# Optimization experiments

Hardware: AMD Instinct MI355X
Metric: run time of the kernel (lower is better)

Reference implementation:

```python
import jax, jax.numpy as jnp
import numpy as np
from jax import lax

Z_DIM, X_DIM, Y_DIM, H_DIM = 128, 64, 64, 512


def setup_inputs() -> dict:
    key = jax.random.key(0)
    ks = jax.random.split(key, 10)
    s = 1.0 / np.sqrt(H_DIM)
    inp = {
        "z": jax.random.normal(ks[0], (1024, Z_DIM), dtype=jnp.float32),
        "x": jax.random.normal(ks[1], (1024, 32, X_DIM), dtype=jnp.float32),
        # LSTM params (PyTorch layout: gates ordered i,f,g,o)
        "W_ih": jax.random.uniform(ks[2], (4 * H_DIM, X_DIM), jnp.float32, -s, s),
        "W_hh": jax.random.uniform(ks[3], (4 * H_DIM, H_DIM), jnp.float32, -s, s),
        "b_ih": jax.random.uniform(ks[4], (4 * H_DIM,), jnp.float32, -s, s),
        "b_hh": jax.random.uniform(ks[5], (4 * H_DIM,), jnp.float32, -s, s),
        # proj_network: z_dim -> hidden
        "W_proj": jax.random.uniform(ks[6], (H_DIM, Z_DIM), jnp.float32, -s, s),
        "b_proj": jax.random.uniform(ks[7], (H_DIM,), jnp.float32, -s, s),
        # projout_network: hidden -> y_dim
        "W_out": jax.random.uniform(ks[8], (Y_DIM, H_DIM), jnp.float32, -s, s),
        "b_out": jax.random.uniform(ks[9], (Y_DIM,), jnp.float32, -s, s),
        "y_pred_len": 128,
    }
    return inp


def reference(z, x, W_ih, W_hh, b_ih, b_hh, W_proj, b_proj, W_out, b_out, y_pred_len):
    # initial recurrent state: h0 = c0 = proj(z)  [B, H]
    h0 = z @ W_proj.T + b_proj
    c0 = h0
    y_prev0 = x[:, -1, :]  # [B, X_DIM]

    def step(carry, _):
        h, c, y_prev = carry
        gates = y_prev @ W_ih.T + b_ih + h @ W_hh.T + b_hh  # [B, 4H]
        i, f, g, o = jnp.split(gates, 4, axis=-1)
        i = jax.nn.sigmoid(i)
        f = jax.nn.sigmoid(f)
        g = jnp.tanh(g)
        o = jax.nn.sigmoid(o)
        c = f * c + i * g
        h = o * jnp.tanh(c)
        y_cur = y_prev + (h @ W_out.T + b_out)  # residual (inference: feed back)
        return (h, c, y_cur), y_cur

    _, ys = lax.scan(step, (h0, c0, y_prev0), None, length=y_pred_len)
    return jnp.transpose(ys, (1, 0, 2))  # [B, T, Y_DIM]
```

## Files before the change

### kernel.cpp

```cpp
#include <hip/hip_runtime.h>
#include <stdint.h>

typedef _Float16 half8 __attribute__((ext_vector_type(8)));
typedef __attribute__((ext_vector_type(4))) float f4;
typedef __attribute__((ext_vector_type(4))) unsigned int u32x4;
typedef __attribute__((ext_vector_type(2))) unsigned int u32x2;

#define LDAH 200
#define EXS  36
#define HSTR 40

__device__ __forceinline__ float sigm(float x) { return 1.0f / (1.0f + __expf(-x)); }
__device__ __forceinline__ float tanh_(float x) { return 1.0f - 2.0f / (__expf(2.0f * x) + 1.0f); }


extern "C" __global__ void __launch_bounds__(256) k_wcat(
    const float* __restrict__ Wih, const float* __restrict__ Whh,
    _Float16* __restrict__ WA, _Float16* __restrict__ WB)
{
    int idx = blockIdx.x * 256 + threadIdx.x;
    int n = idx / 576, k = idx % 576;
    float v = (k < 64) ? Wih[n * 64 + k] : Whh[n * 512 + (k - 64)];
    _Float16 b = (_Float16)v;
    WA[idx] = b;
    if (k < 64) WB[idx] = b;
}

extern "C" __global__ void __launch_bounds__(256) k_comb(
    const float* __restrict__ Wih, const float* __restrict__ Whh,
    const float* __restrict__ Wo, _Float16* __restrict__ WB)
{
    int bx = blockIdx.x;
    int n = bx >> 1;
    int kh = ((bx & 1) << 8) + threadIdx.x;
    float acc = Whh[n * 512 + kh];
    #pragma unroll 16
    for (int p = 0; p < 64; ++p)
        acc += Wih[n * 64 + p] * Wo[p * 512 + kh];
    WB[n * 576 + 64 + kh] = (_Float16)acc;
}

extern "C" __global__ void __launch_bounds__(256) k_misc(
    const float* __restrict__ Wo, const float* __restrict__ bih, const float* __restrict__ bhh,
    const float* __restrict__ Wih, const float* __restrict__ bo, const float* __restrict__ x,
    _Float16* __restrict__ WoB, float* __restrict__ b0v, float* __restrict__ b1v,
    float* __restrict__ yf0, float* __restrict__ yf1,
    _Float16* __restrict__ yh0, _Float16* __restrict__ yh1,
    _Float16* __restrict__ yl0, _Float16* __restrict__ yl1)
{
    int idx = blockIdx.x * 256 + threadIdx.x;
    if (idx < 32768) { WoB[idx] = (_Float16)Wo[idx]; return; }
    if (idx < 34816) {
        int n = idx - 32768;
        float b = bih[n] + bhh[n];
        b0v[n] = b;
        float a = b;
        #pragma unroll 16
        for (int p = 0; p < 64; ++p) a += Wih[n * 64 + p] * bo[p];
        b1v[n] = a;
        return;
    }
    if (idx < 100352) {
        int e = idx - 34816;
        int m = e >> 6, nn = e & 63;
        float v = x[m * 2048 + 31 * 64 + nn];
        yf0[e] = v; yf1[e] = v;
        _Float16 hi = (_Float16)v;
        _Float16 lo = (_Float16)(v - (float)hi);
        yh0[e] = hi; yh1[e] = hi;
        yl0[e] = lo; yl1[e] = lo;
    }
}

extern "C" __global__ void __launch_bounds__(256) k_h0(
    const float* __restrict__ z, const float* __restrict__ Wp, const float* __restrict__ bp,
    float* __restrict__ cst, _Float16* __restrict__ hh0, _Float16* __restrict__ hl0)
{
    int bx = blockIdx.x;
    int m = bx >> 1;
    int n = ((bx & 1) << 8) + threadIdx.x;
    float acc = bp[n];
    const f4* zr = (const f4*)&z[m * 128];
    const f4* wr = (const f4*)&Wp[n * 128];
    #pragma unroll 8
    for (int p = 0; p < 32; ++p) {
        f4 zv = zr[p], wv = wr[p];
        acc += zv[0]*wv[0] + zv[1]*wv[1] + zv[2]*wv[2] + zv[3]*wv[3];
    }
    cst[m * 512 + n] = acc;
    _Float16 hi = (_Float16)acc;
    hh0[m * 512 + n] = hi;
    hl0[m * 512 + n] = (_Float16)(acc - (float)hi);
}


__device__ __forceinline__ void resolve_y(
    int t, int row, int c4,
    const float* __restrict__ yf_in, float* __restrict__ yf_out,
    const float* __restrict__ dl_in, const float* __restrict__ bout,
    _Float16* __restrict__ yh_out, _Float16* __restrict__ yl_out,
    float* __restrict__ out)
{
    f4 a = *(const f4*)&yf_in[row * 64 + c4];
    a += *(const f4*)&bout[c4];
    #pragma unroll
    for (int sp = 0; sp < 16; ++sp)
        a += *(const f4*)&dl_in[sp * 65536 + row * 64 + c4];
    *(f4*)&yf_out[row * 64 + c4] = a;
    *(f4*)&out[row * 8192 + (t - 1) * 64 + c4] = a;
    _Float16 hi4[4], lo4[4];
    #pragma unroll
    for (int x = 0; x < 4; ++x) {
        hi4[x] = (_Float16)a[x];
        lo4[x] = (_Float16)(a[x] - (float)hi4[x]);
    }
    *(u32x2*)&yh_out[row * 64 + c4] = *(u32x2*)hi4;
    *(u32x2*)&yl_out[row * 64 + c4] = *(u32x2*)lo4;
}

extern "C" __global__ void __launch_bounds__(512, 2) k_step(
    int t,
    const _Float16* __restrict__ Wcat,
    const float* __restrict__ bias,
    const _Float16* __restrict__ Wout,
    const float* __restrict__ bout,
    const _Float16* __restrict__ hh_in, const _Float16* __restrict__ hl_in,
    _Float16* __restrict__ hh_out, _Float16* __restrict__ hl_out,
    float* __restrict__ cst,
    const float* __restrict__ yf_in, float* __restrict__ yf_out,
    const _Float16* __restrict__ yh_in, _Float16* __restrict__ yh_out,
    const _Float16* __restrict__ yl_in, _Float16* __restrict__ yl_out,
    const float* __restrict__ dl_in, float* __restrict__ dl_out,
    float* __restrict__ out)
{
    __shared__ __align__(16) unsigned char smem[61440];
    _Float16* sAh = (_Float16*)smem;
    _Float16* sAl = (_Float16*)(smem + 25600);
    float*    sEx = (float*)smem;
    _Float16* sHh = (_Float16*)(smem + 51200);
    _Float16* sHl = (_Float16*)(smem + 56320);

    const int tid = threadIdx.x;
    const int bx  = blockIdx.x;
    const int mt  = bx >> 4, s = bx & 15;
    const int m0  = mt * 64, j0 = s * 32;

    if (t >= 128) {
        if (tid < 64) {
            int row = m0 + s * 4 + (tid >> 4);
            int c4  = (tid & 15) * 4;
            resolve_y(t, row, c4, yf_in, yf_out, dl_in, bout, yh_out, yl_out, out);
        }
        return;
    }

    const int w = tid >> 6, lane = tid & 63, l15 = lane & 15, quad = lane >> 4;
    const int quad8 = quad * 8;
    const int q = w >> 1, hx = w & 1;

    const int cm = tid >> 3, cjb = (tid & 7) * 4;
    const int cjcol = j0 + cjb;
    const int ccrow = (m0 + cm) * 512 + cjcol;
    f4 cpre = *(const f4*)&cst[ccrow];
    f4 bi0 = *(const f4*)&bias[       cjcol];
    f4 bi1 = *(const f4*)&bias[ 512 + cjcol];
    f4 bi2 = *(const f4*)&bias[1024 + cjcol];
    f4 bi3 = *(const f4*)&bias[1536 + cjcol];
    const int dn = w >> 1, ap = w & 1;
    half8 bw = *(const half8*)&Wout[(dn * 16 + l15) * 512 + j0 + quad8];

    const int brow = (q * 512 + j0 + hx * 16 + l15) * 576;

    half8 bv[2][6];
    #pragma unroll
    for (int kc = 0; kc < 6; ++kc)
        bv[0][kc] = *(const half8*)&Wcat[brow + kc * 32 + quad8];

    int rr[3], cc3[3];
    #pragma unroll
    for (int it = 0; it < 3; ++it) {
        int i4 = it * 512 + tid;
        rr[it]  = i4 / 24;
        cc3[it] = (i4 % 24) * 8;
    }

    #pragma unroll
    for (int it = 0; it < 3; ++it) {
        int r = rr[it], cc = cc3[it];
        const _Float16 *sh, *sl;
        if (cc < 64) { sh = &yh_in[(m0 + r) * 64 + cc];         sl = &yl_in[(m0 + r) * 64 + cc]; }
        else         { sh = &hh_in[(m0 + r) * 512 + (cc - 64)]; sl = &hl_in[(m0 + r) * 512 + (cc - 64)]; }
        *(u32x4*)&sAh[r * LDAH + cc] = *(const u32x4*)sh;
        *(u32x4*)&sAl[r * LDAH + cc] = *(const u32x4*)sl;
    }

    f4 zero = {0.0f, 0.0f, 0.0f, 0.0f};
    f4 acc[4];
    acc[0] = zero; acc[1] = zero; acc[2] = zero; acc[3] = zero;

    u32x4 regH[3], regL[3];
    #pragma unroll
    for (int ch = 0; ch < 3; ++ch) {
        if (ch < 2) {
            #pragma unroll
            for (int it = 0; it < 3; ++it) {
                int c = (ch + 1) * 192 + cc3[it] - 64;
                regH[it] = *(const u32x4*)&hh_in[(m0 + rr[it]) * 512 + c];
                regL[it] = *(const u32x4*)&hl_in[(m0 + rr[it]) * 512 + c];
            }
            #pragma unroll
            for (int kc = 0; kc < 6; ++kc)
                bv[(ch + 1) & 1][kc] = *(const half8*)&Wcat[brow + (ch + 1) * 192 + kc * 32 + quad8];
        }
        __syncthreads();
        #pragma unroll
        for (int kc = 0; kc < 6; ++kc) {
            int kq = kc * 32 + quad8;
            half8 b = bv[ch & 1][kc];
            #pragma unroll
            for (int a = 0; a < 4; ++a) {
                half8 ah = *(const half8*)&sAh[(l15 + a * 16) * LDAH + kq];
                acc[a] = __builtin_amdgcn_mfma_f32_16x16x32_f16(ah, b, acc[a], 0, 0, 0);
            }
            #pragma unroll
            for (int a = 0; a < 4; ++a) {
                half8 al = *(const half8*)&sAl[(l15 + a * 16) * LDAH + kq];
                acc[a] = __builtin_amdgcn_mfma_f32_16x16x32_f16(al, b, acc[a], 0, 0, 0);
            }
        }
        if (ch < 2) {
            __syncthreads();
            #pragma unroll
            for (int it = 0; it < 3; ++it) {
                *(u32x4*)&sAh[rr[it] * LDAH + cc3[it]] = regH[it];
                *(u32x4*)&sAl[rr[it] * LDAH + cc3[it]] = regL[it];
            }
        }
    }
    __syncthreads();

    #pragma unroll
    for (int a = 0; a < 4; ++a)
        #pragma unroll
        for (int r = 0; r < 4; ++r)
            sEx[(q * 64 + a * 16 + quad * 4 + r) * EXS + hx * 16 + l15] = acc[a][r];
    __syncthreads();

    {
        f4 c0 = cpre;
        f4 gI = *(const f4*)&sEx[(0 * 64 + cm) * EXS + cjb];
        f4 gF = *(const f4*)&sEx[(1 * 64 + cm) * EXS + cjb];
        f4 gG = *(const f4*)&sEx[(2 * 64 + cm) * EXS + cjb];
        f4 gO = *(const f4*)&sEx[(3 * 64 + cm) * EXS + cjb];
        _Float16 hi4[4], lo4[4];
        #pragma unroll
        for (int x = 0; x < 4; ++x) {
            float iv = sigm(gI[x] + bi0[x]);
            float fv = sigm(gF[x] + bi1[x]);
            float gv = tanh_(gG[x] + bi2[x]);
            float ov = sigm(gO[x] + bi3[x]);
            float cn = fv * c0[x] + iv * gv;
            float hn = ov * tanh_(cn);
            c0[x] = cn;
            _Float16 hi = (_Float16)hn;
            hi4[x] = hi;
            lo4[x] = (_Float16)(hn - (float)hi);
        }
        *(f4*)&cst[ccrow] = c0;
        *(u32x2*)&hh_out[ccrow]        = *(u32x2*)hi4;
        *(u32x2*)&hl_out[ccrow]        = *(u32x2*)lo4;
        *(u32x2*)&sHh[cm * HSTR + cjb] = *(u32x2*)hi4;
        *(u32x2*)&sHl[cm * HSTR + cjb] = *(u32x2*)lo4;
    }
    __syncthreads();

    {
        f4 d[2];
        d[0] = zero; d[1] = zero;
        #pragma unroll
        for (int a2 = 0; a2 < 2; ++a2) {
            int a = ap * 2 + a2;
            half8 ahh = *(const half8*)&sHh[(a * 16 + l15) * HSTR + quad8];
            half8 ahl = *(const half8*)&sHl[(a * 16 + l15) * HSTR + quad8];
            d[a2] = __builtin_amdgcn_mfma_f32_16x16x32_f16(ahh, bw, d[a2], 0, 0, 0);
            d[a2] = __builtin_amdgcn_mfma_f32_16x16x32_f16(ahl, bw, d[a2], 0, 0, 0);
        }
        #pragma unroll
        for (int a2 = 0; a2 < 2; ++a2) {
            int a = ap * 2 + a2;
            #pragma unroll
            for (int r = 0; r < 4; ++r)
                dl_out[s * 65536 + (m0 + a * 16 + quad * 4 + r) * 64 + dn * 16 + l15] = d[a2][r];
        }
    }

    if (t >= 1 && tid < 64) {
        int row = m0 + s * 4 + (tid >> 4);
        int c4  = (tid & 15) * 4;
        resolve_y(t, row, c4, yf_in, yf_out, dl_in, bout, yh_out, yl_out, out);
    }
}

extern "C" void kernel_launch(void* const* d_in, const int* in_sizes, int n_in,
                              void* d_out, int out_size, void* d_ws, size_t ws_size,
                              hipStream_t stream)
{
    const float* z   = (const float*)d_in[0];
    const float* x   = (const float*)d_in[1];
    const float* Wih = (const float*)d_in[2];
    const float* Whh = (const float*)d_in[3];
    const float* bih = (const float*)d_in[4];
    const float* bhh = (const float*)d_in[5];
    const float* Wp  = (const float*)d_in[6];
    const float* bp  = (const float*)d_in[7];
    const float* Wo  = (const float*)d_in[8];
    const float* bo  = (const float*)d_in[9];

    char* w = (char*)d_ws;
    _Float16* WA  = (_Float16*)w; w += 2359296;
    _Float16* WB  = (_Float16*)w; w += 2359296;
    _Float16* WoB = (_Float16*)w; w += 65536;
    float* b0v = (float*)w; w += 8192;
    float* b1v = (float*)w; w += 8192;
    _Float16* hh[2];
    hh[0] = (_Float16*)w; w += 1048576;
    hh[1] = (_Float16*)w; w += 1048576;
    _Float16* hl[2];
    hl[0] = (_Float16*)w; w += 1048576;
    hl[1] = (_Float16*)w; w += 1048576;
    float* cst = (float*)w; w += 2097152;
    float* yf[2];
    yf[0] = (float*)w; w += 262144;
    yf[1] = (float*)w; w += 262144;
    _Float16* yh[2];
    yh[0] = (_Float16*)w; w += 131072;
    yh[1] = (_Float16*)w; w += 131072;
    _Float16* yl[2];
    yl[0] = (_Float16*)w; w += 131072;
    yl[1] = (_Float16*)w; w += 131072;
    float* dl[2];
    dl[0] = (float*)w; w += 4194304;
    dl[1] = (float*)w; w += 4194304;
    float* out = (float*)d_out;

    k_wcat<<<4608, 256, 0, stream>>>(Wih, Whh, WA, WB);
    k_comb<<<4096, 256, 0, stream>>>(Wih, Whh, Wo, WB);
    k_misc<<<392, 256, 0, stream>>>(Wo, bih, bhh, Wih, bo, x, WoB, b0v, b1v,
                                    yf[0], yf[1], yh[0], yh[1], yl[0], yl[1]);
    k_h0<<<2048, 256, 0, stream>>>(z, Wp, bp, cst, hh[0], hl[0]);

    for (int t = 0; t <= 128; ++t) {
        k_step<<<256, 512, 0, stream>>>(t,
            (t == 0) ? WA : WB, (t == 0) ? b0v : b1v,
            WoB, bo,
            hh[t & 1], hl[t & 1], hh[(t + 1) & 1], hl[(t + 1) & 1],
            cst,
            yf[t & 1], yf[(t + 1) & 1],
            yh[t & 1], yh[(t + 1) & 1],
            yl[t & 1], yl[(t + 1) & 1],
            dl[(t + 1) & 1], dl[t & 1],
            out);
    }
}
```

Measured before the change: 2.183 ms.

## Split step kernel into 512 narrower blocks with XCD-aware tile mapping

Halves the hidden-column slice per block (32 to 16) and the threads per block (512 to 256), doubling the grid to 512 blocks so more of the device's compute units are occupied. Block indices are remapped so the row tiles for one batch slice stay on the same XCD, which should improve L2 reuse of the shared activation reads. The y-resolve step is moved to the start of the kernel. The trade-off is that each block now reloads the full 64-row activation tile for half the output columns, and the partial-output buffer doubles to 32 slices that resolve_y must sum.

```diff
diff --git a/kernel.cpp b/kernel.cpp
--- a/kernel.cpp
+++ b/kernel.cpp
@@ -7,8 +7,8 @@
 typedef __attribute__((ext_vector_type(2))) unsigned int u32x2;
 
 #define LDAH 200
-#define EXS  36
-#define HSTR 40
+#define EXS2 20
+#define HST2 24
 
 __device__ __forceinline__ float sigm(float x) { return 1.0f / (1.0f + __expf(-x)); }
 __device__ __forceinline__ float tanh_(float x) { return 1.0f - 2.0f / (__expf(2.0f * x) + 1.0f); }
@@ -95,16 +95,16 @@
 
 
 __device__ __forceinline__ void resolve_y(
-    int t, int row, int c4,
+    int t, int row, int c4, f4 bo4,
     const float* __restrict__ yf_in, float* __restrict__ yf_out,
-    const float* __restrict__ dl_in, const float* __restrict__ bout,
+    const float* __restrict__ dl_in,
     _Float16* __restrict__ yh_out, _Float16* __restrict__ yl_out,
     float* __restrict__ out)
 {
     f4 a = *(const f4*)&yf_in[row * 64 + c4];
-    a += *(const f4*)&bout[c4];
-    #pragma unroll
-    for (int sp = 0; sp < 16; ++sp)
+    a += bo4;
+    #pragma unroll
+    for (int sp = 0; sp < 32; ++sp)
         a += *(const f4*)&dl_in[sp * 65536 + row * 64 + c4];
     *(f4*)&yf_out[row * 64 + c4] = a;
     *(f4*)&out[row * 8192 + (t - 1) * 64 + c4] = a;
@@ -118,7 +118,7 @@
     *(u32x2*)&yl_out[row * 64 + c4] = *(u32x2*)lo4;
 }
 
-extern "C" __global__ void __launch_bounds__(512, 2) k_step(
+extern "C" __global__ void __launch_bounds__(256, 2) k_step(
     int t,
     const _Float16* __restrict__ Wcat,
     const float* __restrict__ bias,
@@ -133,32 +133,32 @@
     const float* __restrict__ dl_in, float* __restrict__ dl_out,
     float* __restrict__ out)
 {
-    __shared__ __align__(16) unsigned char smem[61440];
+    __shared__ __align__(16) unsigned char smem[57344];
     _Float16* sAh = (_Float16*)smem;
     _Float16* sAl = (_Float16*)(smem + 25600);
     float*    sEx = (float*)smem;
     _Float16* sHh = (_Float16*)(smem + 51200);
-    _Float16* sHl = (_Float16*)(smem + 56320);
+    _Float16* sHl = (_Float16*)(smem + 54272);
 
     const int tid = threadIdx.x;
     const int bx  = blockIdx.x;
-    const int mt  = bx >> 4, s = bx & 15;
-    const int m0  = mt * 64, j0 = s * 32;
-
-    if (t >= 128) {
-        if (tid < 64) {
-            int row = m0 + s * 4 + (tid >> 4);
-            int c4  = (tid & 15) * 4;
-            resolve_y(t, row, c4, yf_in, yf_out, dl_in, bout, yh_out, yl_out, out);
-        }
-        return;
-    }
-
-    const int w = tid >> 6, lane = tid & 63, l15 = lane & 15, quad = lane >> 4;
+    const int xcd = bx & 7, slot = bx >> 3;
+    const int mt  = xcd * 2 + (slot >> 5);
+    const int s   = slot & 31;
+    const int m0  = mt * 64, j0 = s * 16;
+
+    if (t >= 1 && tid < 32) {
+        int row = m0 + s * 2 + (tid >> 4);
+        int c4  = (tid & 15) * 4;
+        f4 bo4 = *(const f4*)&bout[c4];
+        resolve_y(t, row, c4, bo4, yf_in, yf_out, dl_in, yh_out, yl_out, out);
+    }
+    if (t >= 128) return;
+
+    const int wv = tid >> 6, lane = tid & 63, l15 = lane & 15, quad = lane >> 4;
     const int quad8 = quad * 8;
-    const int q = w >> 1, hx = w & 1;
-
-    const int cm = tid >> 3, cjb = (tid & 7) * 4;
+
+    const int cm = tid >> 2, cjb = (tid & 3) * 4;
     const int cjcol = j0 + cjb;
     const int ccrow = (m0 + cm) * 512 + cjcol;
     f4 cpre = *(const f4*)&cst[ccrow];
@@ -166,27 +166,26 @@
     f4 bi1 = *(const f4*)&bias[ 512 + cjcol];
     f4 bi2 = *(const f4*)&bias[1024 + cjcol];
     f4 bi3 = *(const f4*)&bias[1536 + cjcol];
-    const int dn = w >> 1, ap = w & 1;
-    half8 bw = *(const half8*)&Wout[(dn * 16 + l15) * 512 + j0 + quad8];
-
-    const int brow = (q * 512 + j0 + hx * 16 + l15) * 576;
+    half8 bw = *(const half8*)&Wout[(wv * 16 + l15) * 512 + j0 + (quad & 1) * 8];
+
+    const int brow = (wv * 512 + j0 + l15) * 576;
 
     half8 bv[2][6];
     #pragma unroll
     for (int kc = 0; kc < 6; ++kc)
         bv[0][kc] = *(const half8*)&Wcat[brow + kc * 32 + quad8];
 
-    int rr[3], cc3[3];
-    #pragma unroll
-    for (int it = 0; it < 3; ++it) {
-        int i4 = it * 512 + tid;
+    int rr[6], cc6[6];
+    #pragma unroll
+    for (int it = 0; it < 6; ++it) {
+        int i4 = it * 256 + tid;
         rr[it]  = i4 / 24;
-        cc3[it] = (i4 % 24) * 8;
-    }
-
-    #pragma unroll
-    for (int it = 0; it < 3; ++it) {
-        int r = rr[it], cc = cc3[it];
+        cc6[it] = (i4 % 24) * 8;
+    }
+
+    #pragma unroll
+    for (int it = 0; it < 6; ++it) {
+        int r = rr[it], cc = cc6[it];
         const _Float16 *sh, *sl;
         if (cc < 64) { sh = &yh_in[(m0 + r) * 64 + cc];         sl = &yl_in[(m0 + r) * 64 + cc]; }
         else         { sh = &hh_in[(m0 + r) * 512 + (cc - 64)]; sl = &hl_in[(m0 + r) * 512 + (cc - 64)]; }
@@ -198,13 +197,13 @@
     f4 acc[4];
     acc[0] = zero; acc[1] = zero; acc[2] = zero; acc[3] = zero;
 
-    u32x4 regH[3], regL[3];
+    u32x4 regH[6], regL[6];
     #pragma unroll
     for (int ch = 0; ch < 3; ++ch) {
         if (ch < 2) {
             #pragma unroll
-            for (int it = 0; it < 3; ++it) {
-                int c = (ch + 1) * 192 + cc3[it] - 64;
+            for (int it = 0; it < 6; ++it) {
+                int c = (ch + 1) * 192 + cc6[it] - 64;
                 regH[it] = *(const u32x4*)&hh_in[(m0 + rr[it]) * 512 + c];
                 regL[it] = *(const u32x4*)&hl_in[(m0 + rr[it]) * 512 + c];
             }
@@ -231,9 +230,9 @@
         if (ch < 2) {
             __syncthreads();
             #pragma unroll
-            for (int it = 0; it < 3; ++it) {
-                *(u32x4*)&sAh[rr[it] * LDAH + cc3[it]] = regH[it];
-                *(u32x4*)&sAl[rr[it] * LDAH + cc3[it]] = regL[it];
+            for (int it = 0; it < 6; ++it) {
+                *(u32x4*)&sAh[rr[it] * LDAH + cc6[it]] = regH[it];
+                *(u32x4*)&sAl[rr[it] * LDAH + cc6[it]] = regL[it];
             }
         }
     }
@@ -243,15 +242,15 @@
     for (int a = 0; a < 4; ++a)
         #pragma unroll
         for (int r = 0; r < 4; ++r)
-            sEx[(q * 64 + a * 16 + quad * 4 + r) * EXS + hx * 16 + l15] = acc[a][r];
+            sEx[(wv * 64 + a * 16 + quad * 4 + r) * EXS2 + l15] = acc[a][r];
     __syncthreads();
 
     {
         f4 c0 = cpre;
-        f4 gI = *(const f4*)&sEx[(0 * 64 + cm) * EXS + cjb];
-        f4 gF = *(const f4*)&sEx[(1 * 64 + cm) * EXS + cjb];
-        f4 gG = *(const f4*)&sEx[(2 * 64 + cm) * EXS + cjb];
-        f4 gO = *(const f4*)&sEx[(3 * 64 + cm) * EXS + cjb];
+        f4 gI = *(const f4*)&sEx[(0 * 64 + cm) * EXS2 + cjb];
+        f4 gF = *(const f4*)&sEx[(1 * 64 + cm) * EXS2 + cjb];
+        f4 gG = *(const f4*)&sEx[(2 * 64 + cm) * EXS2 + cjb];
+        f4 gO = *(const f4*)&sEx[(3 * 64 + cm) * EXS2 + cjb];
         _Float16 hi4[4], lo4[4];
         #pragma unroll
         for (int x = 0; x < 4; ++x) {
@@ -269,35 +268,26 @@
         *(f4*)&cst[ccrow] = c0;
         *(u32x2*)&hh_out[ccrow]        = *(u32x2*)hi4;
         *(u32x2*)&hl_out[ccrow]        = *(u32x2*)lo4;
-        *(u32x2*)&sHh[cm * HSTR + cjb] = *(u32x2*)hi4;
-        *(u32x2*)&sHl[cm * HSTR + cjb] = *(u32x2*)lo4;
+        *(u32x2*)&sHh[cm * HST2 + cjb] = *(u32x2*)hi4;
+        *(u32x2*)&sHl[cm * HST2 + cjb] = *(u32x2*)lo4;
     }
     __syncthreads();
 
     {
-        f4 d[2];
-        d[0] = zero; d[1] = zero;
-        #pragma unroll
-        for (int a2 = 0; a2 < 2; ++a2) {
-            int a = ap * 2 + a2;
-            half8 ahh = *(const half8*)&sHh[(a * 16 + l15) * HSTR + quad8];
-            half8 ahl = *(const half8*)&sHl[(a * 16 + l15) * HSTR + quad8];
-            d[a2] = __builtin_amdgcn_mfma_f32_16x16x32_f16(ahh, bw, d[a2], 0, 0, 0);
-            d[a2] = __builtin_amdgcn_mfma_f32_16x16x32_f16(ahl, bw, d[a2], 0, 0, 0);
-        }
-        #pragma unroll
-        for (int a2 = 0; a2 < 2; ++a2) {
-            int a = ap * 2 + a2;
+        const _Float16* hsrc = (quad < 2) ? sHh : sHl;
+        f4 d[4];
+        #pragma unroll
+        for (int a = 0; a < 4; ++a) d[a] = zero;
+        #pragma unroll
+        for (int a = 0; a < 4; ++a) {
+            half8 av = *(const half8*)&hsrc[(a * 16 + l15) * HST2 + (quad & 1) * 8];
+            d[a] = __builtin_amdgcn_mfma_f32_16x16x32_f16(av, bw, d[a], 0, 0, 0);
+        }
+        #pragma unroll
+        for (int a = 0; a < 4; ++a)
             #pragma unroll
             for (int r = 0; r < 4; ++r)
-                dl_out[s * 65536 + (m0 + a * 16 + quad * 4 + r) * 64 + dn * 16 + l15] = d[a2][r];
-        }
-    }
-
-    if (t >= 1 && tid < 64) {
-        int row = m0 + s * 4 + (tid >> 4);
-        int c4  = (tid & 15) * 4;
-        resolve_y(t, row, c4, yf_in, yf_out, dl_in, bout, yh_out, yl_out, out);
+                dl_out[s * 65536 + (m0 + a * 16 + quad * 4 + r) * 64 + wv * 16 + l15] = d[a][r];
     }
 }
 
@@ -339,8 +329,8 @@
     yl[0] = (_Float16*)w; w += 131072;
     yl[1] = (_Float16*)w; w += 131072;
     float* dl[2];
-    dl[0] = (float*)w; w += 4194304;
-    dl[1] = (float*)w; w += 4194304;
+    dl[0] = (float*)w; w += 8388608;
+    dl[1] = (float*)w; w += 8388608;
     float* out = (float*)d_out;
 
     k_wcat<<<4608, 256, 0, stream>>>(Wih, Whh, WA, WB);
@@ -350,7 +340,7 @@
     k_h0<<<2048, 256, 0, stream>>>(z, Wp, bp, cst, hh[0], hl[0]);
 
     for (int t = 0; t <= 128; ++t) {
-        k_step<<<256, 512, 0, stream>>>(t,
+        k_step<<<512, 256, 0, stream>>>(t,
             (t == 0) ? WA : WB, (t == 0) ? b0v : b1v,
             WoB, bo,
             hh[t & 1], hl[t & 1], hh[(t + 1) & 1], hl[(t + 1) & 1],
```

Measured after the change: 2.123 ms. 1.03x faster.
